# Kernel tuning notes

Hardware: AMD Instinct MI355X
Metric: run time of the kernel (lower is better)

The kernel has to match this reference:

```python
import jax, jax.numpy as jnp
import numpy as np

B = 16384      # batch of Monte Carlo paths
N = 100        # time steps
DIM_W = 3
DT = 0.01
SQRT_DT = DT ** 0.5
SIGMA0 = 0.5   # constant diffusion coefficient (concrete sigma = SIGMA0 * ones(B,1,DIM_W))


def _mlp(x, W1, b1, W2, b2, W3, b3):
    h = jax.nn.relu(x @ W1 + b1)
    h = jax.nn.relu(h @ W2 + b2)
    return h @ W3 + b3


def setup_inputs() -> dict:
    key = jax.random.key(0)
    ks = jax.random.split(key, 8)
    s = 0.1  # modest weight scale for numerical sanity
    return {
        'y0': jnp.ones((1,), jnp.float32),
        'Y0': jnp.zeros((1, 1), jnp.float32),
        'zW1': s * jax.random.normal(ks[0], (2, 64), jnp.float32),
        'zb1': jnp.zeros((64,), jnp.float32),
        'zW2': s * jax.random.normal(ks[1], (64, 64), jnp.float32),
        'zb2': jnp.zeros((64,), jnp.float32),
        'zW3': s * jax.random.normal(ks[2], (64, 3), jnp.float32),
        'zb3': jnp.zeros((3,), jnp.float32),
        'qW1': s * jax.random.normal(ks[3], (2, 64), jnp.float32),
        'qb1': jnp.zeros((64,), jnp.float32),
        'qW2': s * jax.random.normal(ks[4], (64, 64), jnp.float32),
        'qb2': jnp.zeros((64,), jnp.float32),
        'qW3': s * jax.random.normal(ks[5], (64, 1), jnp.float32),
        'qb3': jnp.zeros((1,), jnp.float32),
        'dW': jax.random.normal(ks[6], (N, B, DIM_W), jnp.float32),
        'dZ': jax.random.normal(ks[7], (N, B, DIM_W), jnp.float32),
    }


def reference(y0, Y0, zW1, zb1, zW2, zb2, zW3, zb3,
              qW1, qb1, qW2, qb2, qW3, qb3, dW, dZ):
    y = jnp.broadcast_to(y0.reshape(1, 1), (B, 1))          # (B,1) state
    Y = jnp.broadcast_to(Y0, (B, 1))                         # (B,1) value process
    t = jnp.zeros((B, 1), jnp.float32)

    def step(carry, noise):
        y, Y, t, loss_acc = carry
        dWi, dZi = noise
        inp = jnp.concatenate([t, y], axis=1)                # (B,2)
        z = _mlp(inp, zW1, zb1, zW2, zb2, zW3, zb3)          # (B,3)
        q = _mlp(inp, qW1, qb1, qW2, qb2, qW3, qb3)          # (B,1)
        f = 0.5 * q * q                                      # generator (B,1)
        dw = dWi * SQRT_DT
        dz = dZi * SQRT_DT
        # sigma = SIGMA0 * ones(B,1,DIM_W); bmm(sigma, dw) = SIGMA0 * sum_j dw_j
        diffusion = SIGMA0 * jnp.sum(dw, axis=1, keepdims=True)
        y_new = y + q * DT + diffusion                       # mu = q
        Y_next = Y - f * DT + jnp.sum(z * dw, axis=1, keepdims=True)
        residual = Y_next - (Y - f * DT + jnp.sum(z * dz, axis=1, keepdims=True))
        loss_acc = loss_acc + jnp.mean(residual * residual)
        return (y_new, Y_next, t + DT, loss_acc), None

    (y, Y, t, total_residual_loss), _ = jax.lax.scan(
        step, (y, Y, t, jnp.float32(0.0)), (dW, dZ))
    terminal = y * y                                         # terminal_cost(y)
    terminal_loss = jnp.mean((Y - terminal) ** 2)
    return terminal_loss + total_residual_loss
```

## Files before the change

### kernel.cpp

```cpp
#include <hip/hip_runtime.h>
#include <hip/hip_bf16.h>

#define BATCH   16384
#define NSTEPS  100
#define DT_     0.01f
#define SQRTDT  0.1f
#define SIGMA0_ 0.5f

typedef _Float16  f16x2  __attribute__((ext_vector_type(2)));
typedef _Float16  f16x4  __attribute__((ext_vector_type(4)));
typedef _Float16  f16x8  __attribute__((ext_vector_type(8)));
typedef __fp16    h16x2  __attribute__((ext_vector_type(2)));
typedef float     f32x4  __attribute__((ext_vector_type(4)));

typedef const __attribute__((address_space(1))) void* gas_ptr;
typedef __attribute__((address_space(3))) void*       las_ptr;

__global__ void zero_out_kernel(float* out) { if (threadIdx.x == 0) out[0] = 0.0f; }

static __device__ __forceinline__ f16x4 pk4(const f32x4& d) {
    union { h16x2 h[2]; f16x4 v; } c;
    c.h[0] = __builtin_amdgcn_cvt_pkrtz(d[0], d[1]);
    c.h[1] = __builtin_amdgcn_cvt_pkrtz(d[2], d[3]);
    return c.v;
}

__launch_bounds__(256, 2)
__global__ void deepbsde_kernel(
    const float* __restrict__ y0,  const float* __restrict__ Y0,
    const float* __restrict__ zW1, const float* __restrict__ zb1,
    const float* __restrict__ zW2, const float* __restrict__ zb2,
    const float* __restrict__ zW3, const float* __restrict__ zb3,
    const float* __restrict__ qW1, const float* __restrict__ qb1,
    const float* __restrict__ qW2, const float* __restrict__ qb2,
    const float* __restrict__ qW3, const float* __restrict__ qb3,
    const float* __restrict__ dW,  const float* __restrict__ dZ,
    float* __restrict__ out)
{
    __shared__ __align__(16) char zring[2][8][384];
    __shared__ __align__(16) char qring[2][8][192];
    __shared__ __align__(16) _Float16 tbl[NSTEPS * 128];
    __shared__ float yring[2][NSTEPS + 1][16];
    __shared__ float ffin[2][16];
    __shared__ int   flags[2][2];

    const int tid  = threadIdx.x;
    const int lane = tid & 63;
    const int w    = tid >> 6;
    const int g    = w & 1;
    const bool isQ = (w >= 2);
    const int ln15 = lane & 15, q4 = lane >> 4;
    const int gw   = (blockIdx.x << 1) + g;
    const int pbase = gw << 4;

    if (tid < 4) ((int*)flags)[tid] = 0;

    auto fillz = [&](int i) {
        if (lane < 24) {
            const char* gp = (lane < 12)
                ? (const char*)dW + ((size_t)i * BATCH + pbase) * 12 + (size_t)lane * 16
                : (const char*)dZ + ((size_t)i * BATCH + pbase) * 12 + (size_t)(lane - 12) * 16;
            __builtin_amdgcn_global_load_lds((gas_ptr)gp, (las_ptr)&zring[g][i & 7][0],
                                             16, 0, 0);
        }
    };
    auto fillq = [&](int i) {
        if (lane < 12) {
            const char* gp = (const char*)dW + ((size_t)i * BATCH + pbase) * 12 + (size_t)lane * 16;
            __builtin_amdgcn_global_load_lds((gas_ptr)gp, (las_ptr)&qring[g][i & 7][0],
                                             16, 0, 0);
        }
    };
    if (!isQ) { fillz(0); fillz(1); fillz(2); fillz(3); }
    else      { fillq(0); fillq(1); fillq(2); fillq(3); }

    {
        float tt = 0.0f;
        for (int i = 0; i < NSTEPS; ++i) {
            int r = (tid - (i << 6)) & 255;
            if (r < 64) {
                int q4e = r >> 4, mlp_ = (r >> 3) & 1, m = r & 7;
                const float* Wp = mlp_ ? qW1 : zW1;
                const float* bp = mlp_ ? qb1 : zb1;
                int i0 = 2*m, i1 = 2*m + 1;
                int k0 = 32*(i0 >> 3) + 8*q4e + (i0 & 7);
                int k1 = 32*(i1 >> 3) + 8*q4e + (i1 & 7);
                _Float16 th = (_Float16)tt;
                f16x2 A = {(_Float16)Wp[k0], (_Float16)Wp[k1]};
                f16x2 C = {(_Float16)bp[k0], (_Float16)bp[k1]};
                f16x2 tv = {th, th};
                f16x2 v = A*tv + C;
                int idx = (i*4 + q4e)*16 + mlp_*8 + m;
                *(f16x2*)&tbl[idx << 1] = v;
            }
            tt += DT_;
        }
    }

    const float* W1p = isQ ? qW1 : zW1;
    const float* W2p = isQ ? qW2 : zW2;
    const float* b2p = isQ ? qb2 : zb2;

    f16x2 B1[8];
#pragma unroll
    for (int m = 0; m < 8; ++m) {
        int i0 = 2*m, i1 = 2*m + 1;
        int k0 = 32*(i0 >> 3) + 8*q4 + (i0 & 7);
        int k1 = 32*(i1 >> 3) + 8*q4 + (i1 & 7);
        B1[m] = (f16x2){(_Float16)W1p[64 + k0], (_Float16)W1p[64 + k1]};
    }

    f16x8 Af[4][2];
#pragma unroll
    for (int tN = 0; tN < 4; ++tN)
#pragma unroll
        for (int f = 0; f < 2; ++f)
#pragma unroll
            for (int j = 0; j < 8; ++j) {
                int k = 32*f + 8*q4 + j, n = 16*tN + ln15;
                Af[tN][f][j] = (_Float16)W2p[k*64 + n];
            }

    f32x4 b2v[4];
#pragma unroll
    for (int tN = 0; tN < 4; ++tN)
#pragma unroll
        for (int r = 0; r < 4; ++r)
            b2v[tN][r] = b2p[16*tN + 4*q4 + r];

    const int c3 = ln15 & 3;
    f16x8 A3[2];
#pragma unroll
    for (int fl = 0; fl < 2; ++fl)
#pragma unroll
        for (int j = 0; j < 8; ++j) {
            int tN = 2*fl + (j >> 2);
            int n  = 16*tN + 4*q4 + (j & 3);
            float wv = isQ ? ((c3 == 3) ? qW3[n]                 : 0.0f)
                           : ((c3 < 3)  ? SQRTDT * zW3[n*3 + c3] : 0.0f);
            A3[fl][j] = (_Float16)wv;
        }

    const f32x4 C3b = isQ ? (f32x4){0.0f, 0.0f, 0.0f, qb3[0]}
                          : (f32x4){SQRTDT*zb3[0], SQRTDT*zb3[1], SQRTDT*zb3[2], 0.0f};

    const float CSIG = SIGMA0_ * SQRTDT;
    const float NHDT = -0.5f * DT_;
    const float y0v = y0[0], Y0v = Y0[0];

    const f16x2 zero2h = {(_Float16)0.0f, (_Float16)0.0f};
    const f16x4 zero4h = {(_Float16)0.0f, (_Float16)0.0f, (_Float16)0.0f, (_Float16)0.0f};

    auto mlp = [&](float ycur, f16x8 t0, f16x8 t1) -> f32x4 {
        _Float16 yh = (_Float16)ycur;
        const f16x2 yv = {yh, yh};
        union U8 { f16x8 v; f16x2 h[4]; };
        U8 T0; T0.v = t0; U8 T1; T1.v = t1;
        union { f16x2 h[4]; f16x8 v; } b0, b1;
#pragma unroll
        for (int m = 0; m < 4; ++m) {
            b0.h[m] = __builtin_elementwise_max((f16x2)(B1[m]*yv   + T0.h[m]), zero2h);
            b1.h[m] = __builtin_elementwise_max((f16x2)(B1[m+4]*yv + T1.h[m]), zero2h);
        }
        union { f16x4 q[4]; f16x8 o[2]; } Bh;
#pragma unroll
        for (int tN = 0; tN < 4; ++tN) {
            f32x4 d = b2v[tN];
            d = __builtin_amdgcn_mfma_f32_16x16x32_f16(Af[tN][0], b0.v, d, 0, 0, 0);
            d = __builtin_amdgcn_mfma_f32_16x16x32_f16(Af[tN][1], b1.v, d, 0, 0, 0);
            Bh.q[tN] = __builtin_elementwise_max(pk4(d), zero4h);
        }
        f32x4 Pv = C3b;
        Pv = __builtin_amdgcn_mfma_f32_16x16x32_f16(A3[0], Bh.o[0], Pv, 0, 0, 0);
        Pv = __builtin_amdgcn_mfma_f32_16x16x32_f16(A3[1], Bh.o[1], Pv, 0, 0, 0);
        return Pv;
    };

    __syncthreads();

    f16x8 c0, c1, d0, d1;

    if (!isQ) {
        float Ysum = 0.0f, acc = 0.0f;
        float ya, yb, yc, yd;
        { const f16x8* tp = (const f16x8*)(tbl + q4*32); c0 = tp[0]; c1 = tp[1]; }

        auto zbody = [&](int i, float ycur, f16x8& t0, f16x8& t1, f16x8& u0, f16x8& u1) {
            const float* sl = (const float*)&zring[g][i & 7][0];
            float nw0 = sl[ln15*3 + 0], nw1 = sl[ln15*3 + 1], nw2 = sl[ln15*3 + 2];
            float nz0 = sl[48 + ln15*3 + 0], nz1 = sl[48 + ln15*3 + 1], nz2 = sl[48 + ln15*3 + 2];
            int ip = i + 1; ip = (ip > NSTEPS - 1) ? NSTEPS - 1 : ip;
            { const f16x8* tp = (const f16x8*)(tbl + (ip*4 + q4)*32); u0 = tp[0]; u1 = tp[1]; }

            f32x4 P = mlp(ycur, t0, t1);
            float zs0 = P[0], zs1 = P[1], zs2 = P[2];
            float zdw = fmaf(zs2, nw2, fmaf(zs1, nw1, zs0*nw0));
            float zdz = fmaf(zs2, nz2, fmaf(zs1, nz1, zs0*nz0));
            Ysum += zdw;
            float r = zdw - zdz;
            acc = fmaf(r, r, acc);
        };
        auto ybatch = [&](int base) {
            volatile int* qf = &flags[g][0];
            while (*qf < base + 4) { }
            ya = *(volatile float*)&yring[g][base + 1][ln15];
            yb = *(volatile float*)&yring[g][base + 2][ln15];
            yc = *(volatile float*)&yring[g][base + 3][ln15];
            yd = *(volatile float*)&yring[g][base + 4][ln15];
        };

        __builtin_amdgcn_s_waitcnt(0x0F73); fillz(4);
        zbody(0, y0v, c0, c1, d0, d1);
        ybatch(0);
#pragma unroll 1
        for (int b = 0; b < 23; ++b) {
            int i = 4*b;
            __builtin_amdgcn_s_waitcnt(0x0F73); fillz(i + 5);
            zbody(i + 1, ya, d0, d1, c0, c1);
            __builtin_amdgcn_s_waitcnt(0x0F73); fillz(i + 6);
            zbody(i + 2, yb, c0, c1, d0, d1);
            __builtin_amdgcn_s_waitcnt(0x0F73); fillz(i + 7);
            zbody(i + 3, yc, d0, d1, c0, c1);
            __builtin_amdgcn_s_waitcnt(0x0F73); fillz(i + 8);
            zbody(i + 4, yd, c0, c1, d0, d1);
            ybatch(i + 4);
        }
        __builtin_amdgcn_s_waitcnt(0x0F73); fillz(97);
        zbody(93, ya, d0, d1, c0, c1);
        __builtin_amdgcn_s_waitcnt(0x0F73); fillz(98);
        zbody(94, yb, c0, c1, d0, d1);
        __builtin_amdgcn_s_waitcnt(0x0F73); fillz(99);
        zbody(95, yc, d0, d1, c0, c1);
        __builtin_amdgcn_s_waitcnt(0x0F73);
        zbody(96, yd, c0, c1, d0, d1);
        ybatch(96);
        __builtin_amdgcn_s_waitcnt(0x0F72);
        zbody(97, ya, d0, d1, c0, c1);
        __builtin_amdgcn_s_waitcnt(0x0F71);
        zbody(98, yb, c0, c1, d0, d1);
        __builtin_amdgcn_s_waitcnt(0x0F70);
        zbody(99, yc, d0, d1, c0, c1);

        {
            volatile int* qf = &flags[g][0];
            while (*qf < NSTEPS + 1) { }
        }
        float Fq  = *(volatile float*)&ffin[g][ln15];
        float Yvf = Y0v + Fq + Ysum;
        float yT  = yd;
        float dterm = Yvf - yT*yT;
        acc = fmaf(dterm, dterm, acc);

        float val = (q4 == 0) ? acc : 0.0f;
#pragma unroll
        for (int off = 1; off < 64; off <<= 1) val += __shfl_xor(val, off);
        if (lane == 0) atomicAdd(out, val * (1.0f / BATCH));
    } else {
        float y = y0v, Facc = 0.0f;
        { const f16x8* tp = (const f16x8*)(tbl + q4*32); c0 = tp[2]; c1 = tp[3]; }

        auto qbody = [&](int j, f16x8& t0, f16x8& t1, f16x8& u0, f16x8& u1) {
            const float* sl = (const float*)&qring[g][j & 7][0];
            float nw0 = sl[ln15*3 + 0], nw1 = sl[ln15*3 + 1], nw2 = sl[ln15*3 + 2];
            int jp = j + 1; jp = (jp > NSTEPS - 1) ? NSTEPS - 1 : jp;
            { const f16x8* tp = (const f16x8*)(tbl + (jp*4 + q4)*32); u0 = tp[2]; u1 = tp[3]; }

            f32x4 P = mlp(y, t0, t1);
            float qv = P[3];
            float snw = (nw0 + nw1) + nw2;
            Facc = fmaf(NHDT*qv, qv, Facc);
            y = fmaf(CSIG, snw, fmaf(qv, DT_, y));
            if (q4 == 0) *(volatile float*)&yring[g][j + 1][ln15] = y;
        };

#pragma unroll 1
        for (int jb = 0; jb < 24; ++jb) {
            int j = 4*jb;
            __builtin_amdgcn_s_waitcnt(0x0F73); fillq(j + 4);
            qbody(j,     c0, c1, d0, d1);
            __builtin_amdgcn_s_waitcnt(0x0F73); fillq(j + 5);
            qbody(j + 1, d0, d1, c0, c1);
            __builtin_amdgcn_s_waitcnt(0x0F73); fillq(j + 6);
            qbody(j + 2, c0, c1, d0, d1);
            __builtin_amdgcn_s_waitcnt(0x0F73); fillq(j + 7);
            qbody(j + 3, d0, d1, c0, c1);
            __builtin_amdgcn_s_waitcnt(0xC07F);
            if (lane == 0) *(volatile int*)&flags[g][0] = j + 4;
        }
        __builtin_amdgcn_s_waitcnt(0x0F73);
        qbody(96, c0, c1, d0, d1);
        __builtin_amdgcn_s_waitcnt(0x0F72);
        qbody(97, d0, d1, c0, c1);
        __builtin_amdgcn_s_waitcnt(0x0F71);
        qbody(98, c0, c1, d0, d1);
        __builtin_amdgcn_s_waitcnt(0x0F70);
        qbody(99, d0, d1, c0, c1);
        __builtin_amdgcn_s_waitcnt(0xC07F);
        if (lane == 0) *(volatile int*)&flags[g][0] = NSTEPS;

        if (q4 == 0) *(volatile float*)&ffin[g][ln15] = Facc;
        __builtin_amdgcn_s_waitcnt(0xC07F);
        if (lane == 0) *(volatile int*)&flags[g][0] = NSTEPS + 1;
    }
}

extern "C" void kernel_launch(void* const* d_in, const int* in_sizes, int n_in,
                              void* d_out, int out_size, void* d_ws, size_t ws_size,
                              hipStream_t stream)
{
    zero_out_kernel<<<1, 64, 0, stream>>>((float*)d_out);
    deepbsde_kernel<<<512, 256, 0, stream>>>(
        (const float*)d_in[0],  (const float*)d_in[1],
        (const float*)d_in[2],  (const float*)d_in[3],
        (const float*)d_in[4],  (const float*)d_in[5],
        (const float*)d_in[6],  (const float*)d_in[7],
        (const float*)d_in[8],  (const float*)d_in[9],
        (const float*)d_in[10], (const float*)d_in[11],
        (const float*)d_in[12], (const float*)d_in[13],
        (const float*)d_in[14], (const float*)d_in[15],
        (float*)d_out);
}
```

Before: 155.2 us.

## Interleave paired z-MLP steps, prioritize q-wave, and pair z/q waves per SIMD

```diff
diff --git a/kernel.cpp b/kernel.cpp
--- a/kernel.cpp
+++ b/kernel.cpp
@@ -47,8 +47,9 @@
     const int tid  = threadIdx.x;
     const int lane = tid & 63;
     const int w    = tid >> 6;
-    const int g    = w & 1;
-    const bool isQ = (w >= 2);
+    const int g    = w >> 1;
+    const int flip = (((int)blockIdx.x >> 3) ^ ((int)blockIdx.x >> 8)) & 1;
+    const bool isQ = ((w & 1) ^ flip) != 0;
     const int ln15 = lane & 15, q4 = lane >> 4;
     const int gw   = (blockIdx.x << 1) + g;
     const int pbase = gw << 4;
@@ -151,103 +152,103 @@
     const f16x2 zero2h = {(_Float16)0.0f, (_Float16)0.0f};
     const f16x4 zero4h = {(_Float16)0.0f, (_Float16)0.0f, (_Float16)0.0f, (_Float16)0.0f};
 
-    auto mlp = [&](float ycur, f16x8 t0, f16x8 t1) -> f32x4 {
-        _Float16 yh = (_Float16)ycur;
-        const f16x2 yv = {yh, yh};
-        union U8 { f16x8 v; f16x2 h[4]; };
-        U8 T0; T0.v = t0; U8 T1; T1.v = t1;
-        union { f16x2 h[4]; f16x8 v; } b0, b1;
-#pragma unroll
-        for (int m = 0; m < 4; ++m) {
-            b0.h[m] = __builtin_elementwise_max((f16x2)(B1[m]*yv   + T0.h[m]), zero2h);
-            b1.h[m] = __builtin_elementwise_max((f16x2)(B1[m+4]*yv + T1.h[m]), zero2h);
-        }
-        union { f16x4 q[4]; f16x8 o[2]; } Bh;
-#pragma unroll
-        for (int tN = 0; tN < 4; ++tN) {
-            f32x4 d = b2v[tN];
-            d = __builtin_amdgcn_mfma_f32_16x16x32_f16(Af[tN][0], b0.v, d, 0, 0, 0);
-            d = __builtin_amdgcn_mfma_f32_16x16x32_f16(Af[tN][1], b1.v, d, 0, 0, 0);
-            Bh.q[tN] = __builtin_elementwise_max(pk4(d), zero4h);
-        }
-        f32x4 Pv = C3b;
-        Pv = __builtin_amdgcn_mfma_f32_16x16x32_f16(A3[0], Bh.o[0], Pv, 0, 0, 0);
-        Pv = __builtin_amdgcn_mfma_f32_16x16x32_f16(A3[1], Bh.o[1], Pv, 0, 0, 0);
-        return Pv;
-    };
+    if (isQ && q4 == 0) *(volatile float*)&yring[g][0][ln15] = y0v;
 
     __syncthreads();
-
-    f16x8 c0, c1, d0, d1;
 
     if (!isQ) {
         float Ysum = 0.0f, acc = 0.0f;
         float ya, yb, yc, yd;
-        { const f16x8* tp = (const f16x8*)(tbl + q4*32); c0 = tp[0]; c1 = tp[1]; }
-
-        auto zbody = [&](int i, float ycur, f16x8& t0, f16x8& t1, f16x8& u0, f16x8& u1) {
-            const float* sl = (const float*)&zring[g][i & 7][0];
-            float nw0 = sl[ln15*3 + 0], nw1 = sl[ln15*3 + 1], nw2 = sl[ln15*3 + 2];
-            float nz0 = sl[48 + ln15*3 + 0], nz1 = sl[48 + ln15*3 + 1], nz2 = sl[48 + ln15*3 + 2];
-            int ip = i + 1; ip = (ip > NSTEPS - 1) ? NSTEPS - 1 : ip;
-            { const f16x8* tp = (const f16x8*)(tbl + (ip*4 + q4)*32); u0 = tp[0]; u1 = tp[1]; }
-
-            f32x4 P = mlp(ycur, t0, t1);
-            float zs0 = P[0], zs1 = P[1], zs2 = P[2];
-            float zdw = fmaf(zs2, nw2, fmaf(zs1, nw1, zs0*nw0));
-            float zdz = fmaf(zs2, nz2, fmaf(zs1, nz1, zs0*nz0));
-            Ysum += zdw;
-            float r = zdw - zdz;
-            acc = fmaf(r, r, acc);
-        };
+
         auto ybatch = [&](int base) {
             volatile int* qf = &flags[g][0];
             while (*qf < base + 4) { }
-            ya = *(volatile float*)&yring[g][base + 1][ln15];
-            yb = *(volatile float*)&yring[g][base + 2][ln15];
-            yc = *(volatile float*)&yring[g][base + 3][ln15];
-            yd = *(volatile float*)&yring[g][base + 4][ln15];
+            ya = *(volatile float*)&yring[g][base + 0][ln15];
+            yb = *(volatile float*)&yring[g][base + 1][ln15];
+            yc = *(volatile float*)&yring[g][base + 2][ln15];
+            yd = *(volatile float*)&yring[g][base + 3][ln15];
         };
 
-        __builtin_amdgcn_s_waitcnt(0x0F73); fillz(4);
-        zbody(0, y0v, c0, c1, d0, d1);
-        ybatch(0);
+        auto zpair = [&](int iA, float yA, int iB, float yB) {
+            const float* sA = (const float*)&zring[g][iA & 7][0];
+            const float* sB = (const float*)&zring[g][iB & 7][0];
+            float aw0 = sA[ln15*3+0], aw1 = sA[ln15*3+1], aw2 = sA[ln15*3+2];
+            float az0 = sA[48+ln15*3+0], az1 = sA[48+ln15*3+1], az2 = sA[48+ln15*3+2];
+            float bw0 = sB[ln15*3+0], bw1 = sB[ln15*3+1], bw2 = sB[ln15*3+2];
+            float bz0_ = sB[48+ln15*3+0], bz1_ = sB[48+ln15*3+1], bz2_ = sB[48+ln15*3+2];
+
+            const f16x8* tpA = (const f16x8*)(tbl + (iA*4 + q4)*32);
+            const f16x8* tpB = (const f16x8*)(tbl + (iB*4 + q4)*32);
+            union U8 { f16x8 v; f16x2 h[4]; };
+            U8 TA0; TA0.v = tpA[0]; U8 TA1; TA1.v = tpA[1];
+            U8 TB0; TB0.v = tpB[0]; U8 TB1; TB1.v = tpB[1];
+
+            _Float16 yhA = (_Float16)yA, yhB = (_Float16)yB;
+            const f16x2 yvA = {yhA, yhA}, yvB = {yhB, yhB};
+            union { f16x2 h[4]; f16x8 v; } a0, a1, b0, b1;
+#pragma unroll
+            for (int m = 0; m < 4; ++m) {
+                a0.h[m] = __builtin_elementwise_max((f16x2)(B1[m]*yvA   + TA0.h[m]), zero2h);
+                b0.h[m] = __builtin_elementwise_max((f16x2)(B1[m]*yvB   + TB0.h[m]), zero2h);
+                a1.h[m] = __builtin_elementwise_max((f16x2)(B1[m+4]*yvA + TA1.h[m]), zero2h);
+                b1.h[m] = __builtin_elementwise_max((f16x2)(B1[m+4]*yvB + TB1.h[m]), zero2h);
+            }
+
+            union { f16x4 q[4]; f16x8 o[2]; } BA, BB;
+#pragma unroll
+            for (int tN = 0; tN < 4; ++tN) {
+                f32x4 dA = b2v[tN];
+                f32x4 dB = b2v[tN];
+                dA = __builtin_amdgcn_mfma_f32_16x16x32_f16(Af[tN][0], a0.v, dA, 0, 0, 0);
+                dB = __builtin_amdgcn_mfma_f32_16x16x32_f16(Af[tN][0], b0.v, dB, 0, 0, 0);
+                dA = __builtin_amdgcn_mfma_f32_16x16x32_f16(Af[tN][1], a1.v, dA, 0, 0, 0);
+                dB = __builtin_amdgcn_mfma_f32_16x16x32_f16(Af[tN][1], b1.v, dB, 0, 0, 0);
+                BA.q[tN] = __builtin_elementwise_max(pk4(dA), zero4h);
+                BB.q[tN] = __builtin_elementwise_max(pk4(dB), zero4h);
+            }
+
+            f32x4 PA = C3b, PB = C3b;
+            PA = __builtin_amdgcn_mfma_f32_16x16x32_f16(A3[0], BA.o[0], PA, 0, 0, 0);
+            PB = __builtin_amdgcn_mfma_f32_16x16x32_f16(A3[0], BB.o[0], PB, 0, 0, 0);
+            PA = __builtin_amdgcn_mfma_f32_16x16x32_f16(A3[1], BA.o[1], PA, 0, 0, 0);
+            PB = __builtin_amdgcn_mfma_f32_16x16x32_f16(A3[1], BB.o[1], PB, 0, 0, 0);
+
+            float zdwA = fmaf(PA[2], aw2, fmaf(PA[1], aw1, PA[0]*aw0));
+            float zdzA = fmaf(PA[2], az2, fmaf(PA[1], az1, PA[0]*az0));
+            Ysum += zdwA;
+            float rA = zdwA - zdzA;
+            acc = fmaf(rA, rA, acc);
+            float zdwB = fmaf(PB[2], bw2, fmaf(PB[1], bw1, PB[0]*bw0));
+            float zdzB = fmaf(PB[2], bz2_, fmaf(PB[1], bz1_, PB[0]*bz0_));
+            Ysum += zdwB;
+            float rB = zdwB - zdzB;
+            acc = fmaf(rB, rB, acc);
+        };
+
 #pragma unroll 1
-        for (int b = 0; b < 23; ++b) {
+        for (int b = 0; b < 24; ++b) {
             int i = 4*b;
-            __builtin_amdgcn_s_waitcnt(0x0F73); fillz(i + 5);
-            zbody(i + 1, ya, d0, d1, c0, c1);
-            __builtin_amdgcn_s_waitcnt(0x0F73); fillz(i + 6);
-            zbody(i + 2, yb, c0, c1, d0, d1);
-            __builtin_amdgcn_s_waitcnt(0x0F73); fillz(i + 7);
-            zbody(i + 3, yc, d0, d1, c0, c1);
-            __builtin_amdgcn_s_waitcnt(0x0F73); fillz(i + 8);
-            zbody(i + 4, yd, c0, c1, d0, d1);
-            ybatch(i + 4);
-        }
-        __builtin_amdgcn_s_waitcnt(0x0F73); fillz(97);
-        zbody(93, ya, d0, d1, c0, c1);
-        __builtin_amdgcn_s_waitcnt(0x0F73); fillz(98);
-        zbody(94, yb, c0, c1, d0, d1);
-        __builtin_amdgcn_s_waitcnt(0x0F73); fillz(99);
-        zbody(95, yc, d0, d1, c0, c1);
-        __builtin_amdgcn_s_waitcnt(0x0F73);
-        zbody(96, yd, c0, c1, d0, d1);
+            ybatch(i);
+            __builtin_amdgcn_s_waitcnt(0x0F72);
+            fillz(i + 4); fillz(i + 5);
+            zpair(i,     ya, i + 1, yb);
+            __builtin_amdgcn_s_waitcnt(0x0F72);
+            fillz(i + 6); fillz(i + 7);
+            zpair(i + 2, yc, i + 3, yd);
+        }
         ybatch(96);
         __builtin_amdgcn_s_waitcnt(0x0F72);
-        zbody(97, ya, d0, d1, c0, c1);
-        __builtin_amdgcn_s_waitcnt(0x0F71);
-        zbody(98, yb, c0, c1, d0, d1);
+        zpair(96, ya, 97, yb);
         __builtin_amdgcn_s_waitcnt(0x0F70);
-        zbody(99, yc, d0, d1, c0, c1);
+        zpair(98, yc, 99, yd);
 
         {
             volatile int* qf = &flags[g][0];
             while (*qf < NSTEPS + 1) { }
         }
-        float Fq  = *(volatile float*)&ffin[g][ln15];
+        float Fq = *(volatile float*)&ffin[g][ln15];
+        float yT = *(volatile float*)&yring[g][NSTEPS][ln15];
         float Yvf = Y0v + Fq + Ysum;
-        float yT  = yd;
         float dterm = Yvf - yT*yT;
         acc = fmaf(dterm, dterm, acc);
 
@@ -256,7 +257,9 @@
         for (int off = 1; off < 64; off <<= 1) val += __shfl_xor(val, off);
         if (lane == 0) atomicAdd(out, val * (1.0f / BATCH));
     } else {
+        __builtin_amdgcn_s_setprio(1);
         float y = y0v, Facc = 0.0f;
+        f16x8 c0, c1, d0, d1;
         { const f16x8* tp = (const f16x8*)(tbl + q4*32); c0 = tp[2]; c1 = tp[3]; }
 
         auto qbody = [&](int j, f16x8& t0, f16x8& t1, f16x8& u0, f16x8& u1) {
@@ -265,8 +268,29 @@
             int jp = j + 1; jp = (jp > NSTEPS - 1) ? NSTEPS - 1 : jp;
             { const f16x8* tp = (const f16x8*)(tbl + (jp*4 + q4)*32); u0 = tp[2]; u1 = tp[3]; }
 
-            f32x4 P = mlp(y, t0, t1);
-            float qv = P[3];
+            _Float16 yh = (_Float16)y;
+            const f16x2 yv = {yh, yh};
+            union U8 { f16x8 v; f16x2 h[4]; };
+            U8 T0; T0.v = t0; U8 T1; T1.v = t1;
+            union { f16x2 h[4]; f16x8 v; } b0, b1;
+#pragma unroll
+            for (int m = 0; m < 4; ++m) {
+                b0.h[m] = __builtin_elementwise_max((f16x2)(B1[m]*yv   + T0.h[m]), zero2h);
+                b1.h[m] = __builtin_elementwise_max((f16x2)(B1[m+4]*yv + T1.h[m]), zero2h);
+            }
+            union { f16x4 q[4]; f16x8 o[2]; } Bh;
+#pragma unroll
+            for (int tN = 0; tN < 4; ++tN) {
+                f32x4 d = b2v[tN];
+                d = __builtin_amdgcn_mfma_f32_16x16x32_f16(Af[tN][0], b0.v, d, 0, 0, 0);
+                d = __builtin_amdgcn_mfma_f32_16x16x32_f16(Af[tN][1], b1.v, d, 0, 0, 0);
+                Bh.q[tN] = __builtin_elementwise_max(pk4(d), zero4h);
+            }
+            f32x4 Pv = C3b;
+            Pv = __builtin_amdgcn_mfma_f32_16x16x32_f16(A3[0], Bh.o[0], Pv, 0, 0, 0);
+            Pv = __builtin_amdgcn_mfma_f32_16x16x32_f16(A3[1], Bh.o[1], Pv, 0, 0, 0);
+
+            float qv = Pv[3];
             float snw = (nw0 + nw1) + nw2;
             Facc = fmaf(NHDT*qv, qv, Facc);
             y = fmaf(CSIG, snw, fmaf(qv, DT_, y));
```

New measurement: 155.8 us. About the same (+0.4%).
